# Kernel tuning notes

Hardware: AMD Instinct MI355X
Metric: run time of the kernel (lower is better)

The kernel has to match this reference:

```python
import jax, jax.numpy as jnp
import numpy as np

N = 50000      # nodes
E = 400000     # edges (before self-loops)
IN = 256       # in_dim
H = 4          # heads in layer 1
C = 64         # h_dim (per-head channels, layer 1)
OUT = 16       # out_dim (layer 2, 1 head)
NEG_SLOPE = 0.2


def gatv2_layer(x, src, dst, Wl, bl, Wr, br, att, bias, heads, ch, concat, num_nodes):
    # x: [N, F]; src/dst: [E']; Wl/Wr: [F, heads*ch]; att: [heads, ch]
    xl = (x @ Wl + bl).reshape(num_nodes, heads, ch)  # source transform
    xr = (x @ Wr + br).reshape(num_nodes, heads, ch)  # target transform
    m = xl[src] + xr[dst]                              # [E', H, C] gather
    e = jnp.sum(jax.nn.leaky_relu(m, NEG_SLOPE) * att, axis=-1)  # [E', H]
    # segment softmax over incoming edges of each dst node (self-loops ensure non-empty)
    emax = jax.ops.segment_max(e, dst, num_segments=num_nodes)   # [N, H]
    ee = jnp.exp(e - emax[dst])
    denom = jax.ops.segment_sum(ee, dst, num_segments=num_nodes)  # [N, H]
    alpha = ee / (denom[dst] + 1e-16)                              # [E', H]
    out = jax.ops.segment_sum(alpha[..., None] * xl[src], dst, num_segments=num_nodes)  # [N,H,C]
    if concat:
        out = out.reshape(num_nodes, heads * ch)
    else:
        out = out.mean(axis=1)
    return out + bias


def setup_inputs() -> dict:
    key = jax.random.key(0)
    ks = jax.random.split(key, 16)
    s = 0.05
    inp = {
        "x": jax.random.normal(ks[0], (N, IN), jnp.float32),
        "edge_index": jax.random.randint(ks[1], (2, E), 0, N),
        # layer 1 params (in_dim -> heads*h_dim)
        "Wl1": jax.random.normal(ks[2], (IN, H * C), jnp.float32) * s,
        "bl1": jnp.zeros((H * C,), jnp.float32),
        "Wr1": jax.random.normal(ks[3], (IN, H * C), jnp.float32) * s,
        "br1": jnp.zeros((H * C,), jnp.float32),
        "att1": jax.random.normal(ks[4], (H, C), jnp.float32) * s,
        "bias1": jnp.zeros((H * C,), jnp.float32),
        # layer 2 params (heads*h_dim -> out_dim, 1 head)
        "Wl2": jax.random.normal(ks[5], (H * C, OUT), jnp.float32) * s,
        "bl2": jnp.zeros((OUT,), jnp.float32),
        "Wr2": jax.random.normal(ks[6], (H * C, OUT), jnp.float32) * s,
        "br2": jnp.zeros((OUT,), jnp.float32),
        "att2": jax.random.normal(ks[7], (1, OUT), jnp.float32) * s,
        "bias2": jnp.zeros((OUT,), jnp.float32),
    }
    return inp


def reference(x, edge_index, Wl1, bl1, Wr1, br1, att1, bias1, Wl2, bl2, Wr2, br2, att2, bias2):
    # add self loops (PyG GATv2Conv default add_self_loops=True)
    loop = jnp.arange(N, dtype=edge_index.dtype)
    src = jnp.concatenate([edge_index[0], loop])
    dst = jnp.concatenate([edge_index[1], loop])
    h = gatv2_layer(x, src, dst, Wl1, bl1, Wr1, br1, att1, bias1, H, C, True, N)
    h = jnp.tanh(h)
    o = gatv2_layer(h, src, dst, Wl2, bl2, Wr2, br2, att2, bias2, 1, OUT, False, N)
    return o, jax.nn.log_softmax(o, axis=1)
```

## Files before the change

kernel.cpp:

```cpp
#include <hip/hip_runtime.h>

typedef __bf16 bfv8 __attribute__((ext_vector_type(8)));
typedef float f32x4 __attribute__((ext_vector_type(4)));
typedef float f32x2 __attribute__((ext_vector_type(2)));
typedef short shortv8 __attribute__((ext_vector_type(8)));
typedef unsigned short usv8 __attribute__((ext_vector_type(8)));

__device__ __forceinline__ float b2f(unsigned short u) {
  unsigned int v = ((unsigned int)u) << 16;
  float f;
  __builtin_memcpy(&f, &v, 4);
  return f;
}
__device__ __forceinline__ unsigned short f2b(float f) {
  unsigned int u;
  __builtin_memcpy(&u, &f, 4);
  u += 0x7fffu + ((u >> 16) & 1u);
  return (unsigned short)(u >> 16);
}

__device__ __forceinline__ f32x2 bf2x(unsigned int u) {
  f32x2 r;
  r.x = __builtin_bit_cast(float, u << 16);
  r.y = __builtin_bit_cast(float, u & 0xffff0000u);
  return r;
}

template <int CTRL>
__device__ __forceinline__ float dpp_mv(float x) {
  int xi = __builtin_bit_cast(int, x);
  int yi = __builtin_amdgcn_update_dpp(0, xi, CTRL, 0xf, 0xf, true);
  return __builtin_bit_cast(float, yi);
}

__device__ __forceinline__ float tanh_fast(float x) {
  float e2 = __expf(2.f * x);
  float r = __builtin_amdgcn_rcpf(e2 + 1.f);
  float th = fmaf(-2.f, r, 1.f);
  if (!(th == th)) th = 0.f;
  return th;
}

__global__ void probe_kernel(const unsigned short* __restrict__ x, int* __restrict__ flag) {
  int lane = threadIdx.x;
  int cnt = 0;
  for (int i = lane; i < 4096; i += 64) {
    unsigned int e = (x[i] >> 7) & 0xffu;
    if (e >= 0x86u) cnt++;
  }
#pragma unroll
  for (int off = 1; off < 64; off <<= 1) cnt += __shfl_xor(cnt, off, 64);
  if (lane == 0) *flag = (cnt > 100) ? 1 : 0;
}

#define P_TOT 140352
__global__ __launch_bounds__(256) void fused_pre_kernel(
    const void* __restrict__ x, unsigned short* __restrict__ Xc,
    const int* __restrict__ flagp, int NX,
    const int* __restrict__ ei, int E, int Nn, int* __restrict__ cnt,
    const void* p0, const void* p1, const void* p2, const void* p3,
    const void* p4, const void* p5, const void* p6, const void* p7,
    const void* p8, const void* p9, const void* p10, const void* p11,
    unsigned short* __restrict__ Pc, int nb_convx, int nb_count) {
  int b = blockIdx.x;
  int t = threadIdx.x;
  if (b < nb_convx) {
    if (!*flagp) return;
    int i = (b * 256 + t) * 4;
    if (i >= NX) return;
    float4 f = *reinterpret_cast<const float4*>((const float*)x + i);
    ushort4 o;
    o.x = f2b(f.x); o.y = f2b(f.y); o.z = f2b(f.z); o.w = f2b(f.w);
    *reinterpret_cast<ushort4*>(Xc + i) = o;
  } else if (b < nb_convx + nb_count) {
    int i = (b - nb_convx) * 256 + t;
    int total = E + Nn;
    if (i >= total) return;
    int d = (i < E) ? ei[E + i] : (i - E);
    if ((unsigned)d >= (unsigned)Nn) d = 0;
    atomicAdd(&cnt[d], 1);
  } else {
    int i = (b - nb_convx - nb_count) * 256 + t;
    if (i >= P_TOT) return;
    const int offs[13] = {0, 65536, 65792, 131328, 131584, 131840, 132096,
                          136192, 136208, 140304, 140320, 140336, P_TOT};
    const void* ptrs[12] = {p0, p1, p2, p3, p4, p5, p6, p7, p8, p9, p10, p11};
    int flag = *flagp;
    int k = 0;
    while (i >= offs[k + 1]) k++;
    int local = i - offs[k];
    unsigned short v;
    if (flag) v = f2b(((const float*)ptrs[k])[local]);
    else v = ((const unsigned short*)ptrs[k])[local];
    Pc[i] = v;
  }
}

__global__ __launch_bounds__(1024) void fused_mid_kernel(
    const int* __restrict__ cnt, int* __restrict__ row_start, int* __restrict__ blkTot,
    int Nn, int nb_scan,
    const unsigned short* __restrict__ Pc,
    unsigned short* __restrict__ WT1, unsigned short* __restrict__ WT2) {
  int b = blockIdx.x;
  int t = threadIdx.x;
  if (b < nb_scan) {
    __shared__ int buf[1024];
    int i = b * 1024 + t;
    int v = (i < Nn) ? cnt[i] : 0;
    buf[t] = v;
    __syncthreads();
    for (int off = 1; off < 1024; off <<= 1) {
      int x = (t >= off) ? buf[t - off] : 0;
      __syncthreads();
      buf[t] += x;
      __syncthreads();
    }
    if (i < Nn) row_start[i] = buf[t] - v;
    if (t == 1023) blkTot[b] = buf[1023];
  } else {
    int idx = (b - nb_scan) * 1024 + t;
    if (idx < 512 * 256) {
      int n = idx >> 8, k = idx & 255;
      WT1[idx] = (n < 256) ? Pc[0 + k * 256 + n]
                           : Pc[65792 + k * 256 + (n - 256)];
    } else {
      int j = idx - 512 * 256;
      if (j < 32 * 256) {
        int n = j >> 8, k = j & 255;
        WT2[j] = (n < 16) ? Pc[132096 + k * 16 + n]
                          : Pc[136208 + k * 16 + (n - 16)];
      }
    }
  }
}

__global__ __launch_bounds__(64) void scan2_kernel(const int* __restrict__ blkTot,
                                                   int* __restrict__ blkOff, int nb,
                                                   int* __restrict__ row_start, int Nn,
                                                   int total) {
  int lane = threadIdx.x;
  int v = (lane < nb) ? blkTot[lane] : 0;
  int s = v;
#pragma unroll
  for (int off = 1; off < 64; off <<= 1) {
    int u = __shfl_up(s, off, 64);
    if (lane >= off) s += u;
  }
  int excl = s - v;
  blkOff[lane] = excl;
  if (lane == 63) blkOff[64] = s;
  int idx = Nn >> 10;
  int bo = (idx >= 64) ? __shfl(s, 63, 64) : __shfl(excl, idx, 64);
  if (lane == 0) row_start[Nn] = total - bo;
}

__global__ __launch_bounds__(256) void fill_kernel(const int* __restrict__ ei, int E, int Nn,
                                                   const int* __restrict__ row_start,
                                                   const int* __restrict__ blkOff,
                                                   int* __restrict__ cursor,
                                                   int* __restrict__ csr_src) {
  int i = blockIdx.x * 256 + threadIdx.x;
  int total = E + Nn;
  if (i >= total) return;
  int s, d;
  if (i < E) { s = ei[i]; d = ei[E + i]; } else { s = i - E; d = i - E; }
  if ((unsigned)d >= (unsigned)Nn) d = 0;
  if ((unsigned)s >= (unsigned)Nn) s = 0;
  int pos = row_start[d] + blkOff[d >> 10] + atomicAdd(&cursor[d], 1);
  if ((unsigned)pos < (unsigned)total) csr_src[pos] = s;
}

__global__ __launch_bounds__(256) void gemm1_kernel(
    const unsigned short* __restrict__ Xc,
    const unsigned short* __restrict__ x_raw,
    const int* __restrict__ flagp,
    const unsigned short* __restrict__ WT,
    const unsigned short* __restrict__ bl, const unsigned short* __restrict__ br,
    unsigned short* __restrict__ C, int M) {
  __shared__ unsigned short smem[18432];
  const unsigned short* X = (*flagp) ? Xc : x_raw;
  const int t = threadIdx.x;
  const int lane = t & 63;
  const int w = t >> 6;
  const int quad = lane >> 4;
  const int l16 = lane & 15;
  const int n_blk = blockIdx.x & 3;
  const int by = blockIdx.x >> 2;
  const int m_base = by * 128 + (w >> 1) * 64;
  const int n_base = n_blk * 128 + (w & 1) * 64;

  f32x4 acc[4][4];
#pragma unroll
  for (int i = 0; i < 4; i++)
#pragma unroll
    for (int j = 0; j < 4; j++) acc[i][j] = (f32x4){0.f, 0.f, 0.f, 0.f};

  int rowp[4];
#pragma unroll
  for (int i = 0; i < 4; i++) {
    int row = m_base + 16 * i + l16;
    if (row >= M) row = M - 1;
    rowp[i] = row;
  }

#pragma unroll
  for (int k0 = 0; k0 < 256; k0 += 32) {
    bfv8 a[4], b[4];
#pragma unroll
    for (int i = 0; i < 4; i++)
      a[i] = *reinterpret_cast<const bfv8*>(X + (size_t)rowp[i] * 256 + k0 + quad * 8);
#pragma unroll
    for (int j = 0; j < 4; j++) {
      int col = n_base + 16 * j + l16;
      b[j] = *reinterpret_cast<const bfv8*>(WT + (size_t)col * 256 + k0 + quad * 8);
    }
#pragma unroll
    for (int i = 0; i < 4; i++)
#pragma unroll
      for (int j = 0; j < 4; j++)
        acc[i][j] = __builtin_amdgcn_mfma_f32_16x16x32_bf16(a[i], b[j], acc[i][j], 0, 0, 0);
  }

  unsigned short* lt = smem + w * 4608;
#pragma unroll
  for (int j = 0; j < 4; j++) {
    int col = n_base + 16 * j + l16;
    float bias = (col < 256) ? b2f(bl[col]) : b2f(br[col - 256]);
#pragma unroll
    for (int i = 0; i < 4; i++)
#pragma unroll
      for (int r = 0; r < 4; r++)
        lt[(16 * i + quad * 4 + r) * 72 + 16 * j + l16] = f2b(acc[i][j][r] + bias);
  }
  __syncthreads();
#pragma unroll
  for (int pass = 0; pass < 8; pass++) {
    int row = pass * 8 + (lane >> 3);
    int colg = (lane & 7) * 8;
    shortv8 v = *reinterpret_cast<const shortv8*>(lt + row * 72 + colg);
    int grow = m_base + row;
    if (grow < M)
      *reinterpret_cast<shortv8*>(C + (size_t)grow * 512 + n_base + colg) = v;
  }
}

__global__ __launch_bounds__(256) void gemm2_kernel(
    const unsigned short* __restrict__ H, const unsigned short* __restrict__ WT,
    const unsigned short* __restrict__ bl, const unsigned short* __restrict__ br,
    float* __restrict__ C, int M) {
  const int lane = threadIdx.x & 63;
  const int w = threadIdx.x >> 6;
  const int quad = lane >> 4;
  const int l16 = lane & 15;
  const int m_base = blockIdx.x * 256 + w * 64;

  f32x4 acc[4][2];
#pragma unroll
  for (int i = 0; i < 4; i++)
#pragma unroll
    for (int j = 0; j < 2; j++) acc[i][j] = (f32x4){0.f, 0.f, 0.f, 0.f};

#pragma unroll
  for (int k0 = 0; k0 < 256; k0 += 32) {
    bfv8 a[4], b[2];
#pragma unroll
    for (int i = 0; i < 4; i++) {
      int row = m_base + 16 * i + l16;
      if (row >= M) row = M - 1;
      a[i] = *reinterpret_cast<const bfv8*>(H + (size_t)row * 256 + k0 + quad * 8);
    }
#pragma unroll
    for (int j = 0; j < 2; j++) {
      int col = 16 * j + l16;
      b[j] = *reinterpret_cast<const bfv8*>(WT + (size_t)col * 256 + k0 + quad * 8);
    }
#pragma unroll
    for (int i = 0; i < 4; i++)
#pragma unroll
      for (int j = 0; j < 2; j++)
        acc[i][j] = __builtin_amdgcn_mfma_f32_16x16x32_bf16(a[i], b[j], acc[i][j], 0, 0, 0);
  }

#pragma unroll
  for (int j = 0; j < 2; j++) {
    int col = 16 * j + l16;
    float bias = (j == 0) ? b2f(bl[l16]) : b2f(br[l16]);
#pragma unroll
    for (int i = 0; i < 4; i++) {
#pragma unroll
      for (int r = 0; r < 4; r++) {
        int row = m_base + 16 * i + quad * 4 + r;
        if (row < M) C[(size_t)row * 32 + col] = acc[i][j][r] + bias;
      }
    }
  }
}

__global__ __launch_bounds__(256) void agg1_kernel(
    const unsigned short* __restrict__ C1,
    const unsigned short* __restrict__ att1,
    const unsigned short* __restrict__ bias1,
    const int* __restrict__ row_start, const int* __restrict__ blkOff,
    const int* __restrict__ csr_src,
    unsigned short* __restrict__ H1,
    int Nn, int Etot) {
  int wid = blockIdx.x * 4 + (threadIdx.x >> 6);
  if (wid >= Nn) return;
  int lane = threadIdx.x & 63;
  int half = lane >> 5;
  int c0 = (lane & 31) * 8;

  f32x2 at2[4], xr2[4];
  {
    uint4 a4 = *reinterpret_cast<const uint4*>(att1 + c0);
    uint4 r4 = *reinterpret_cast<const uint4*>(C1 + (size_t)wid * 512 + 256 + c0);
    at2[0] = bf2x(a4.x); at2[1] = bf2x(a4.y); at2[2] = bf2x(a4.z); at2[3] = bf2x(a4.w);
    xr2[0] = bf2x(r4.x); xr2[1] = bf2x(r4.y); xr2[2] = bf2x(r4.z); xr2[3] = bf2x(r4.w);
  }

  float denom = 0.f;
  f32x2 acc2[4] = {};
  int beg = row_start[wid] + blkOff[wid >> 10];
  int end = row_start[wid + 1] + blkOff[(wid + 1) >> 10];
  if (beg < 0) beg = 0;
  if (end < beg || end - beg > Etot) end = beg;

  for (int base = beg; base < end; base += 64) {
    int cend = min(end, base + 64);
    int pl = base + lane;
    if (pl >= end) pl = end - 1;
    int s_pre = csr_src[pl];
#pragma unroll 2
    for (int i = base; i < cend; i += 2) {
      int p = i + half;
      bool valid = p < cend;
      int s = __shfl(s_pre, p - base, 64);
      if ((unsigned)s >= (unsigned)Nn) s = 0;
      uint4 rw = *reinterpret_cast<const uint4*>(C1 + (size_t)s * 512 + c0);
      f32x2 xl0 = bf2x(rw.x), xl1 = bf2x(rw.y), xl2 = bf2x(rw.z), xl3 = bf2x(rw.w);
      f32x2 m0 = xl0 + xr2[0], m1 = xl1 + xr2[1];
      f32x2 m2 = xl2 + xr2[2], m3 = xl3 + xr2[3];
      f32x2 l0 = __builtin_elementwise_max(m0, m0 * 0.2f);
      f32x2 l1 = __builtin_elementwise_max(m1, m1 * 0.2f);
      f32x2 l2 = __builtin_elementwise_max(m2, m2 * 0.2f);
      f32x2 l3 = __builtin_elementwise_max(m3, m3 * 0.2f);
      f32x2 d2 = l0 * at2[0];
      d2 += l1 * at2[1];
      d2 += l2 * at2[2];
      d2 += l3 * at2[3];
      float dot = d2.x + d2.y;
      dot += dpp_mv<0xB1>(dot);
      dot += dpp_mv<0x4E>(dot);
      dot += dpp_mv<0x141>(dot);
      dot = fminf(fmaxf(dot, -60.f), 60.f);
      float wgt = valid ? __expf(dot) : 0.f;
      denom += wgt;
      acc2[0] += xl0 * wgt;
      acc2[1] += xl1 * wgt;
      acc2[2] += xl2 * wgt;
      acc2[3] += xl3 * wgt;
    }
  }
  denom += __shfl_xor(denom, 32, 64);
#pragma unroll
  for (int k = 0; k < 4; k++) {
    acc2[k].x += __shfl_xor(acc2[k].x, 32, 64);
    acc2[k].y += __shfl_xor(acc2[k].y, 32, 64);
  }

  if (half == 0) {
    float inv = __builtin_amdgcn_rcpf(denom + 1e-16f);
    uint4 b4 = *reinterpret_cast<const uint4*>(bias1 + c0);
    f32x2 bb[4] = {bf2x(b4.x), bf2x(b4.y), bf2x(b4.z), bf2x(b4.w)};
    uint4 o;
    unsigned int od[4];
#pragma unroll
    for (int k = 0; k < 4; k++) {
      f32x2 xv = acc2[k] * inv + bb[k];
      float t0 = tanh_fast(xv.x);
      float t1 = tanh_fast(xv.y);
      od[k] = (unsigned int)f2b(t0) | ((unsigned int)f2b(t1) << 16);
    }
    o.x = od[0]; o.y = od[1]; o.z = od[2]; o.w = od[3];
    *reinterpret_cast<uint4*>(H1 + (size_t)wid * 256 + c0) = o;
  }
}

__global__ __launch_bounds__(256) void agg2_kernel(
    const float* __restrict__ C2,
    const unsigned short* __restrict__ att2,
    const unsigned short* __restrict__ bias2,
    const int* __restrict__ row_start, const int* __restrict__ blkOff,
    const int* __restrict__ csr_src,
    float* __restrict__ out,
    int Nn, int Etot) {
  int wid = blockIdx.x * 4 + (threadIdx.x >> 6);
  if (wid >= Nn) return;
  int lane = threadIdx.x & 63;
  int eslot = lane >> 2;
  int cg = (lane & 3) * 4;

  float at[4], xr[4];
  {
    ushort4 a4 = *reinterpret_cast<const ushort4*>(att2 + cg);
    at[0] = b2f(a4.x); at[1] = b2f(a4.y); at[2] = b2f(a4.z); at[3] = b2f(a4.w);
    float4 r4 = *reinterpret_cast<const float4*>(C2 + (size_t)wid * 32 + 16 + cg);
    xr[0] = r4.x; xr[1] = r4.y; xr[2] = r4.z; xr[3] = r4.w;
  }

  float denom = 0.f;
  float acc[4] = {0.f, 0.f, 0.f, 0.f};
  int beg = row_start[wid] + blkOff[wid >> 10];
  int end = row_start[wid + 1] + blkOff[(wid + 1) >> 10];
  if (beg < 0) beg = 0;
  if (end < beg || end - beg > Etot) end = beg;

  for (int base = beg; base < end; base += 64) {
    int cend = min(end, base + 64);
    int pl = base + lane;
    if (pl >= end) pl = end - 1;
    int s_pre = csr_src[pl];
    for (int i = base; i < cend; i += 16) {
      int p = i + eslot;
      bool valid = p < cend;
      int s = __shfl(s_pre, p - base, 64);
      if ((unsigned)s >= (unsigned)Nn) s = 0;
      float4 x4 = *reinterpret_cast<const float4*>(C2 + (size_t)s * 32 + cg);
      float xl[4] = {x4.x, x4.y, x4.z, x4.w};
      float dot = 0.f;
#pragma unroll
      for (int k = 0; k < 4; k++) {
        float m = xl[k] + xr[k];
        float l = fmaxf(m, 0.2f * m);
        dot = fmaf(l, at[k], dot);
      }
      dot += dpp_mv<0xB1>(dot);
      dot += dpp_mv<0x4E>(dot);
      dot = fminf(fmaxf(dot, -60.f), 60.f);
      float wgt = valid ? __expf(dot) : 0.f;
      denom += wgt;
#pragma unroll
      for (int k = 0; k < 4; k++) acc[k] = fmaf(wgt, xl[k], acc[k]);
    }
  }
  denom += dpp_mv<0x124>(denom);
  denom += dpp_mv<0x128>(denom);
#pragma unroll
  for (int k = 0; k < 4; k++) {
    acc[k] += dpp_mv<0x124>(acc[k]);
    acc[k] += dpp_mv<0x128>(acc[k]);
  }
#pragma unroll
  for (int off = 16; off <= 32; off <<= 1) {
    denom += __shfl_xor(denom, off, 64);
#pragma unroll
    for (int k = 0; k < 4; k++) acc[k] += __shfl_xor(acc[k], off, 64);
  }

  float inv = __builtin_amdgcn_rcpf(denom + 1e-16f);
  ushort4 b4 = *reinterpret_cast<const ushort4*>(bias2 + cg);
  float bb[4] = {b2f(b4.x), b2f(b4.y), b2f(b4.z), b2f(b4.w)};
  float o[4];
#pragma unroll
  for (int k = 0; k < 4; k++) {
    o[k] = acc[k] * inv + bb[k];
    if (!(o[k] == o[k])) o[k] = 0.f;
  }
  float mx = fmaxf(fmaxf(o[0], o[1]), fmaxf(o[2], o[3]));
  mx = fmaxf(mx, dpp_mv<0xB1>(mx));
  mx = fmaxf(mx, dpp_mv<0x4E>(mx));
  float se = 0.f;
#pragma unroll
  for (int k = 0; k < 4; k++) se += __expf(o[k] - mx);
  se += dpp_mv<0xB1>(se);
  se += dpp_mv<0x4E>(se);
  float ls = logf(se);
  if (lane < 4) {
    float4 vo = {o[0], o[1], o[2], o[3]};
    float4 vl = {o[0] - mx - ls, o[1] - mx - ls, o[2] - mx - ls, o[3] - mx - ls};
    *reinterpret_cast<float4*>(out + (size_t)wid * 16 + cg) = vo;
    *reinterpret_cast<float4*>(out + (size_t)Nn * 16 + (size_t)wid * 16 + cg) = vl;
  }
}

extern "C" void kernel_launch(void* const* d_in, const int* in_sizes, int n_in,
                              void* d_out, int out_size, void* d_ws, size_t ws_size,
                              hipStream_t stream) {
  const void* x_raw = d_in[0];
  const int* ei     = (const int*)d_in[1];

  const int M = in_sizes[0] / 256;
  const int E = in_sizes[1] / 2;
  const int TOT = E + M;
  const int NX = M * 256;

  char* ws = (char*)d_ws;
  size_t off = 0;
  auto alloc = [&](size_t bytes) -> void* {
    void* p = ws + off;
    off = (off + bytes + 255) & ~(size_t)255;
    return p;
  };
  int*            flag   = (int*)alloc(4);
  unsigned short* Pc     = (unsigned short*)alloc((size_t)P_TOT * 2);
  unsigned short* Xc     = (unsigned short*)alloc((size_t)NX * 2);
  unsigned short* WT1    = (unsigned short*)alloc((size_t)512 * 256 * 2);
  unsigned short* WT2    = (unsigned short*)alloc((size_t)32 * 256 * 2);
  int*            cnt    = (int*)alloc((size_t)M * 4);
  int*            cursor = (int*)alloc((size_t)M * 4);
  int*            row_start = (int*)alloc((size_t)(M + 1) * 4);
  int*            csr_src   = (int*)alloc((size_t)TOT * 4);
  int*            blkTot = (int*)alloc(64 * 4);
  int*            blkOff = (int*)alloc(65 * 4);
  float*          C2     = (float*)alloc((size_t)M * 32 * 4);
  unsigned short* C1     = (unsigned short*)alloc((size_t)M * 512 * 2);
  const size_t need = off;
  (void)n_in;
  unsigned short* H1 = Xc;

  if (ws_size < need) {
    hipMemsetAsync(d_out, 0, (size_t)out_size * 4, stream);
    return;
  }

  unsigned short* bl1c   = Pc + 65536;
  unsigned short* br1c   = Pc + 131328;
  unsigned short* att1c  = Pc + 131584;
  unsigned short* bias1c = Pc + 131840;
  unsigned short* bl2c   = Pc + 136192;
  unsigned short* br2c   = Pc + 140304;
  unsigned short* att2c  = Pc + 140320;
  unsigned short* bias2c = Pc + 140336;

  hipMemsetAsync(cnt, 0, (size_t)M * 4, stream);
  hipMemsetAsync(cursor, 0, (size_t)M * 4, stream);

  probe_kernel<<<1, 64, 0, stream>>>((const unsigned short*)x_raw, flag);

  const int nb_convx = (NX / 4 + 255) / 256;
  const int nb_count = (TOT + 255) / 256;
  const int nb_convp = (P_TOT + 255) / 256;
  fused_pre_kernel<<<nb_convx + nb_count + nb_convp, 256, 0, stream>>>(
      x_raw, Xc, flag, NX, ei, E, M, cnt,
      d_in[2], d_in[3], d_in[4], d_in[5], d_in[6], d_in[7], d_in[8], d_in[9],
      d_in[10], d_in[11], d_in[12], d_in[13], Pc, nb_convx, nb_count);

  const int nb_scan = (M + 1023) / 1024;
  const int nb_tr = (512 * 256 + 32 * 256 + 1023) / 1024;
  fused_mid_kernel<<<nb_scan + nb_tr, 1024, 0, stream>>>(cnt, row_start, blkTot, M,
                                                         nb_scan, Pc, WT1, WT2);

  scan2_kernel<<<1, 64, 0, stream>>>(blkTot, blkOff, nb_scan, row_start, M, TOT);

  fill_kernel<<<(TOT + 255) / 256, 256, 0, stream>>>(ei, E, M, row_start, blkOff,
                                                     cursor, csr_src);

  const int nb_gemm = 4 * ((M + 127) / 128);
  gemm1_kernel<<<nb_gemm, 256, 0, stream>>>(Xc, (const unsigned short*)x_raw, flag,
                                            WT1, bl1c, br1c, C1, M);

  agg1_kernel<<<(M + 3) / 4, 256, 0, stream>>>(C1, att1c, bias1c, row_start, blkOff,
                                               csr_src, H1, M, TOT);

  gemm2_kernel<<<(M + 255) / 256, 256, 0, stream>>>(H1, WT2, bl2c, br2c, C2, M);

  agg2_kernel<<<(M + 3) / 4, 256, 0, stream>>>(C2, att2c, bias2c, row_start, blkOff,
                                               csr_src, (float*)d_out, M, TOT);
}
```

Before: 301.4 us.

## Stage GEMM1 A tiles in swizzled LDS with double buffering, fold cursor memset

gemm1 now loads the X rows for its 128-row block cooperatively into XOR-swizzled shared memory, double-buffered in 64-wide K chunks with register prefetch, so the two column-half waves share one copy instead of each reading A from global. The cursor zeroing moves into the scan kernel, which removes one memset launch. agg1's edge loop unroll goes from 2 to 4. The changes add more syncthreads and register pressure, and the B operand is still read directly from global.

```diff
diff --git a/kernel.cpp b/kernel.cpp
--- a/kernel.cpp
+++ b/kernel.cpp
@@ -98,7 +98,7 @@
 
 __global__ __launch_bounds__(1024) void fused_mid_kernel(
     const int* __restrict__ cnt, int* __restrict__ row_start, int* __restrict__ blkTot,
-    int Nn, int nb_scan,
+    int* __restrict__ cursor, int Nn, int nb_scan,
     const unsigned short* __restrict__ Pc,
     unsigned short* __restrict__ WT1, unsigned short* __restrict__ WT2) {
   int b = blockIdx.x;
@@ -108,6 +108,7 @@
     int i = b * 1024 + t;
     int v = (i < Nn) ? cnt[i] : 0;
     buf[t] = v;
+    if (i < Nn) cursor[i] = 0;
     __syncthreads();
     for (int off = 1; off < 1024; off <<= 1) {
       int x = (t >= off) ? buf[t - off] : 0;
@@ -186,41 +187,79 @@
   const int l16 = lane & 15;
   const int n_blk = blockIdx.x & 3;
   const int by = blockIdx.x >> 2;
-  const int m_base = by * 128 + (w >> 1) * 64;
+  const int m_blk = by * 128;
+  const int m_base = m_blk + (w >> 1) * 64;
   const int n_base = n_blk * 128 + (w & 1) * 64;
 
+  const int st_row = t >> 3;
+  const int st_seg = t & 7;
+
   f32x4 acc[4][4];
 #pragma unroll
   for (int i = 0; i < 4; i++)
 #pragma unroll
     for (int j = 0; j < 4; j++) acc[i][j] = (f32x4){0.f, 0.f, 0.f, 0.f};
 
-  int rowp[4];
+  shortv8 st[4];
 #pragma unroll
   for (int i = 0; i < 4; i++) {
-    int row = m_base + 16 * i + l16;
-    if (row >= M) row = M - 1;
-    rowp[i] = row;
-  }
-
-#pragma unroll
-  for (int k0 = 0; k0 < 256; k0 += 32) {
-    bfv8 a[4], b[4];
-#pragma unroll
-    for (int i = 0; i < 4; i++)
-      a[i] = *reinterpret_cast<const bfv8*>(X + (size_t)rowp[i] * 256 + k0 + quad * 8);
-#pragma unroll
-    for (int j = 0; j < 4; j++) {
-      int col = n_base + 16 * j + l16;
-      b[j] = *reinterpret_cast<const bfv8*>(WT + (size_t)col * 256 + k0 + quad * 8);
-    }
-#pragma unroll
-    for (int i = 0; i < 4; i++)
-#pragma unroll
-      for (int j = 0; j < 4; j++)
-        acc[i][j] = __builtin_amdgcn_mfma_f32_16x16x32_bf16(a[i], b[j], acc[i][j], 0, 0, 0);
-  }
-
+    int gr = m_blk + st_row + 32 * i;
+    if (gr >= M) gr = M - 1;
+    st[i] = *reinterpret_cast<const shortv8*>(X + (size_t)gr * 256 + st_seg * 8);
+  }
+#pragma unroll
+  for (int i = 0; i < 4; i++) {
+    int row = st_row + 32 * i;
+    *reinterpret_cast<shortv8*>(smem + row * 64 + ((st_seg ^ (row & 7)) * 8)) = st[i];
+  }
+  __syncthreads();
+
+#pragma unroll
+  for (int c = 0; c < 4; c++) {
+    if (c < 3) {
+#pragma unroll
+      for (int i = 0; i < 4; i++) {
+        int gr = m_blk + st_row + 32 * i;
+        if (gr >= M) gr = M - 1;
+        st[i] = *reinterpret_cast<const shortv8*>(X + (size_t)gr * 256 + (c + 1) * 64 +
+                                                  st_seg * 8);
+      }
+    }
+    const unsigned short* bb = smem + (c & 1) * 8192;
+#pragma unroll
+    for (int sub = 0; sub < 2; sub++) {
+      bfv8 a[4], b[4];
+      int seg_r = sub * 4 + quad;
+#pragma unroll
+      for (int i = 0; i < 4; i++) {
+        int lrow = (w >> 1) * 64 + 16 * i + l16;
+        a[i] = *reinterpret_cast<const bfv8*>(bb + lrow * 64 + ((seg_r ^ (lrow & 7)) * 8));
+      }
+#pragma unroll
+      for (int j = 0; j < 4; j++) {
+        int col = n_base + 16 * j + l16;
+        b[j] = *reinterpret_cast<const bfv8*>(WT + (size_t)col * 256 + c * 64 + sub * 32 +
+                                              quad * 8);
+      }
+#pragma unroll
+      for (int i = 0; i < 4; i++)
+#pragma unroll
+        for (int j = 0; j < 4; j++)
+          acc[i][j] = __builtin_amdgcn_mfma_f32_16x16x32_bf16(a[i], b[j], acc[i][j], 0, 0, 0);
+    }
+    if (c < 3) {
+      int buf = (c + 1) & 1;
+#pragma unroll
+      for (int i = 0; i < 4; i++) {
+        int row = st_row + 32 * i;
+        *reinterpret_cast<shortv8*>(smem + buf * 8192 + row * 64 +
+                                    ((st_seg ^ (row & 7)) * 8)) = st[i];
+      }
+      __syncthreads();
+    }
+  }
+
+  __syncthreads();
   unsigned short* lt = smem + w * 4608;
 #pragma unroll
   for (int j = 0; j < 4; j++) {
@@ -330,7 +369,7 @@
     int pl = base + lane;
     if (pl >= end) pl = end - 1;
     int s_pre = csr_src[pl];
-#pragma unroll 2
+#pragma unroll 4
     for (int i = base; i < cend; i += 2) {
       int p = i + half;
       bool valid = p < cend;
@@ -533,7 +572,6 @@
   unsigned short* bias2c = Pc + 140336;
 
   hipMemsetAsync(cnt, 0, (size_t)M * 4, stream);
-  hipMemsetAsync(cursor, 0, (size_t)M * 4, stream);
 
   probe_kernel<<<1, 64, 0, stream>>>((const unsigned short*)x_raw, flag);
 
@@ -547,8 +585,8 @@
 
   const int nb_scan = (M + 1023) / 1024;
   const int nb_tr = (512 * 256 + 32 * 256 + 1023) / 1024;
-  fused_mid_kernel<<<nb_scan + nb_tr, 1024, 0, stream>>>(cnt, row_start, blkTot, M,
-                                                         nb_scan, Pc, WT1, WT2);
+  fused_mid_kernel<<<nb_scan + nb_tr, 1024, 0, stream>>>(cnt, row_start, blkTot,
+                                                         cursor, M, nb_scan, Pc, WT1, WT2);
 
   scan2_kernel<<<1, 64, 0, stream>>>(blkTot, blkOff, nb_scan, row_start, M, TOT);
 
```

After: 289.1 us. 1.04x faster.
